# Performance work log

Measured on AMD Instinct MI355X. Metric: run time of the kernel, lower is better.

Reference implementation:

```python
import jax, jax.numpy as jnp
import numpy as np

B, NPG, DIN, ED, DEG = 16, 1024, 16, 8, 32
HEADS, OUT1 = 5, 6
HID = HEADS * OUT1          # 30 features after conv1
C1, C2 = 32, 4              # DIFFPool cluster counts
N = B * NPG                 # 16384 total nodes
E = N * DEG                 # 524288 edges


def _egat_conv(x, src, dst, eattr, W, a_s, a_d, We, heads, outc, n_nodes):
    # Edge-gated GAT: per-edge attention logits from src/dst node features plus
    # a linear projection of edge attributes, segment-softmax over incoming edges.
    h = (x @ W).reshape(n_nodes, heads, outc)
    logit = jax.nn.leaky_relu((h[src] * a_s).sum(-1) + (h[dst] * a_d).sum(-1) + eattr @ We, 0.2)  # [E, heads]
    m = jax.ops.segment_max(logit, dst, num_segments=n_nodes)
    ex = jnp.exp(logit - m[dst])
    den = jax.ops.segment_sum(ex, dst, num_segments=n_nodes)
    alpha = ex / (den[dst] + 1e-16)
    out = jax.ops.segment_sum(alpha[:, :, None] * h[src], dst, num_segments=n_nodes)
    return out.reshape(n_nodes, heads * outc), alpha


def _diff_pool(x, adj, s_logits, b, n, c, d):
    s = jax.nn.softmax(s_logits.reshape(b, n, c), axis=-1)
    xp = jnp.einsum('bnc,bnd->bcd', s, x.reshape(b, n, d))
    adjp = jnp.einsum('bnc,bnm,bmk->bck', s, adj, s)
    reg = jnp.mean((adj - jnp.einsum('bnc,bmc->bnm', s, s)) ** 2)  # link-pred loss
    return xp.reshape(b * c, d), adjp, reg


def _dense_edges(b, c):
    base = jnp.arange(c)
    off = (jnp.arange(b) * c)[:, None]
    src = (jnp.repeat(base, c)[None, :] + off).reshape(-1)
    dst = (jnp.tile(base, c)[None, :] + off).reshape(-1)
    return src, dst


def _forward(x, edge_index, edge_attr, adj, params):
    (W1, a_src1, a_dst1, We1, Wp1, as_p1, ad_p1, Wep1,
     Wp2, as_p2, ad_p2, Wep2, Wf1, bf1, Wf2, bf2) = params
    src, dst = edge_index[0], edge_index[1]
    x1, e = _egat_conv(x, src, dst, edge_attr, W1, a_src1, a_dst1, We1, HEADS, OUT1, N)  # [N,30]
    e_dot = jnp.prod(e, axis=-1)[:, None]  # _EGATConv.dot: product over heads (unused downstream)
    s1, _ = _egat_conv(x1, src, dst, edge_attr, Wp1, as_p1, ad_p1, Wep1, 1, C1, N)
    x2, adj2, reg1 = _diff_pool(x1, adj, s1, B, NPG, C1, HID)
    src2, dst2 = _dense_edges(B, C1)
    ea2 = adj2.reshape(B * C1 * C1, 1)  # pooled graph is dense; adj values as edge attrs
    s2, _ = _egat_conv(x2, src2, dst2, ea2, Wp2, as_p2, ad_p2, Wep2, 1, C2, B * C1)
    x3, _, reg2 = _diff_pool(x2, adj2, s2, B, C1, C2, HID)
    reg = reg1 * 10.0 + reg2 * 0.1
    z = x3.reshape(B, C2 * HID)
    z = jax.nn.relu(z @ Wf1 + bf1)
    logits = z @ Wf2 + bf2
    return logits, reg


def setup_inputs() -> dict:
    key = jax.random.key(0)
    ks = jax.random.split(key, 20)
    # block-diagonal random edges: each graph has NPG*DEG edges within its block
    src_l = jax.random.randint(ks[0], (B, NPG * DEG), 0, NPG)
    dst_l = jax.random.randint(ks[1], (B, NPG * DEG), 0, NPG)
    off = (jnp.arange(B) * NPG)[:, None]
    edge_index = jnp.stack([(src_l + off).reshape(-1), (dst_l + off).reshape(-1)])
    adj = jnp.zeros((B, NPG, NPG), jnp.float32).at[jnp.arange(B)[:, None], src_l, dst_l].set(1.0)
    edge_attr = jax.random.uniform(ks[2], (E, ED), jnp.float32)
    x = jax.random.normal(ks[3], (N, DIN), jnp.float32)
    y = jax.random.randint(ks[4], (B,), 0, 2)

    def nrm(k, shape, fan):
        return jax.random.normal(k, shape, jnp.float32) / np.float32(np.sqrt(fan))

    return dict(
        x=x, edge_index=edge_index, edge_attr=edge_attr, y=y, adj=adj,
        W1=nrm(ks[5], (DIN, HEADS * OUT1), DIN),
        a_src1=nrm(ks[6], (HEADS, OUT1), OUT1),
        a_dst1=nrm(ks[7], (HEADS, OUT1), OUT1),
        We1=nrm(ks[8], (ED, HEADS), ED),
        Wp1=nrm(ks[9], (HID, C1), HID),
        as_p1=nrm(ks[10], (1, C1), C1),
        ad_p1=nrm(ks[11], (1, C1), C1),
        Wep1=nrm(ks[12], (ED, 1), ED),
        Wp2=nrm(ks[13], (HID, C2), HID),
        as_p2=nrm(ks[14], (1, C2), C2),
        ad_p2=nrm(ks[15], (1, C2), C2),
        Wep2=nrm(ks[16], (1, 1), 1),
        Wf1=nrm(ks[17], (C2 * HID, 32), C2 * HID),
        bf1=jnp.zeros((32,), jnp.float32),
        Wf2=nrm(ks[18], (32, 2), 32),
        bf2=jnp.zeros((2,), jnp.float32),
    )


def reference(x, edge_index, edge_attr, y, adj, W1, a_src1, a_dst1, We1, Wp1, as_p1, ad_p1, Wep1, Wp2, as_p2, ad_p2, Wep2, Wf1, bf1, Wf2, bf2):
    params = (W1, a_src1, a_dst1, We1, Wp1, as_p1, ad_p1, Wep1,
              Wp2, as_p2, ad_p2, Wep2, Wf1, bf1, Wf2, bf2)
    return _forward(x, edge_index, edge_attr, adj, params)
```

## Files before the change

kernel.cpp:

```cpp
#include <hip/hip_runtime.h>
#include <math.h>

#define NB 16
#define NPG 1024
#define DIN 16
#define ED 8
#define NHEADS 5
#define OUT1 6
#define HID 30
#define C1 32
#define C2 4
#define NN (NB*NPG)
#define EE (NN*32)
#define EPG 32768
#define CH 16
#define CE 2048

__device__ __forceinline__ float lrelu(float v){ return v >= 0.f ? v : 0.2f*v; }

__device__ __forceinline__ void chunk_gc(int& g, int& c){
    int x = blockIdx.x & 7;
    int j = blockIdx.x >> 3;
    g = x + 8*(j >> 4);
    c = j & 15;
}

__device__ __forceinline__ size_t xcd_chunk_base(){
    int x = blockIdx.x & 7;
    int j = blockIdx.x >> 3;
    int g = x + 8*(j >> 7);
    int c = j & 127;
    return (size_t)g*EPG + (size_t)c*256;
}

__global__ void k_hist_chunk(const int* __restrict__ src, const int* __restrict__ dst,
                             int* __restrict__ histD, int* __restrict__ histS,
                             const float* __restrict__ x, const float* __restrict__ W1,
                             const float* __restrict__ as1, const float* __restrict__ ad1,
                             float* __restrict__ h1, float* __restrict__ hs1, float* __restrict__ hd1){
    int t = threadIdx.x;
    if (blockIdx.x < 256){
        __shared__ int hD[NPG], hS[NPG];
        for (int i = t; i < NPG; i += 256){ hD[i] = 0; hS[i] = 0; }
        __syncthreads();
        int g, c; chunk_gc(g, c);
        size_t e0 = ((size_t)g*CH + c)*CE;
        #pragma unroll
        for (int i = 0; i < 8; i++){
            size_t e = e0 + i*256 + t;
            atomicAdd(&hD[dst[e] & (NPG-1)], 1);
            atomicAdd(&hS[src[e] & (NPG-1)], 1);
        }
        __syncthreads();
        size_t hb = ((size_t)g*CH + c)*NPG;
        for (int i = t; i < NPG; i += 256){
            histD[hb + i] = hD[i];
            histS[hb + i] = hS[i];
        }
        return;
    }
    __shared__ float Ws[DIN*HID];
    __shared__ float as_s[HID], ad_s[HID];
    for (int i = t; i < DIN*HID; i += blockDim.x) Ws[i] = W1[i];
    if (t < HID){ as_s[t] = as1[t]; ad_s[t] = ad1[t]; }
    __syncthreads();
    int n = (blockIdx.x - 256)*blockDim.x + t;
    if (n >= NN) return;
    float xv[DIN];
    #pragma unroll
    for (int i = 0; i < DIN; i++) xv[i] = x[n*DIN + i];
    float hv[HID];
    #pragma unroll
    for (int j = 0; j < HID; j++){
        float a = 0.f;
        #pragma unroll
        for (int i = 0; i < DIN; i++) a += xv[i]*Ws[i*HID + j];
        hv[j] = a; h1[(size_t)n*HID + j] = a;
    }
    #pragma unroll
    for (int h = 0; h < NHEADS; h++){
        float s = 0.f, d = 0.f;
        #pragma unroll
        for (int c2 = 0; c2 < OUT1; c2++){ s += hv[h*OUT1+c2]*as_s[h*OUT1+c2]; d += hv[h*OUT1+c2]*ad_s[h*OUT1+c2]; }
        hs1[n*NHEADS + h] = s; hd1[n*NHEADS + h] = d;
    }
}

__global__ void k_cumhist(int* __restrict__ histD, int* __restrict__ histS,
                          int* __restrict__ deg, int* __restrict__ degS){
    int tid = blockIdx.x*blockDim.x + threadIdx.x;
    int* hist; int* dg;
    if (tid < NN){ hist = histD; dg = deg; }
    else         { hist = histS; dg = degS; tid -= NN; }
    int g = tid >> 10, n = tid & (NPG-1);
    int run = 0;
    #pragma unroll
    for (int c = 0; c < CH; c++){
        size_t idx = ((size_t)g*CH + c)*NPG + n;
        int v = hist[idx];
        hist[idx] = run;
        run += v;
    }
    dg[tid] = run;
}

__global__ __launch_bounds__(1024) void k_scan2f(const int* __restrict__ deg,
                        const int* __restrict__ degS,
                        int* __restrict__ rowptr, int* __restrict__ rowptrS){
    __shared__ int wtot[16];
    __shared__ int wbase[16];
    const int* d = (blockIdx.x == 0) ? deg    : degS;
    int* rp      = (blockIdx.x == 0) ? rowptr : rowptrS;
    int t = threadIdx.x;
    int lane = t & 63, wv = t >> 6;
    int base = t*16;
    int loc[16]; int tot = 0;
    #pragma unroll
    for (int i = 0; i < 16; i++){ loc[i] = tot; tot += d[base + i]; }
    int sincl = tot;
    #pragma unroll
    for (int off = 1; off < 64; off <<= 1){
        int v = __shfl_up(sincl, off, 64);
        if (lane >= off) sincl += v;
    }
    if (lane == 63) wtot[wv] = sincl;
    __syncthreads();
    if (t == 0){
        int run = 0;
        #pragma unroll
        for (int w = 0; w < 16; w++){ wbase[w] = run; run += wtot[w]; }
    }
    __syncthreads();
    int gexcl = wbase[wv] + sincl - tot;
    #pragma unroll
    for (int i = 0; i < 16; i++) rp[base + i] = gexcl + loc[i];
    if (t == 1023) rp[NN] = gexcl + tot;
}

__global__ void k_scatter_det(const int* __restrict__ src, const int* __restrict__ dst,
                              const int* __restrict__ rowptr, const int* __restrict__ rowptrS,
                              const int* __restrict__ histD, const int* __restrict__ histS,
                              int2* __restrict__ se, int* __restrict__ nbrS){
    __shared__ int baseD[NPG], baseS[NPG];
    int t = threadIdx.x;
    int g, c; chunk_gc(g, c);
    size_t hb = ((size_t)g*CH + c)*NPG;
    for (int i = t; i < NPG; i += 256){
        baseD[i] = rowptr[g*NPG + i] + histD[hb + i];
        baseS[i] = rowptrS[g*NPG + i] + histS[hb + i];
    }
    __syncthreads();
    size_t e0 = ((size_t)g*CH + c)*CE;
    #pragma unroll
    for (int i = 0; i < 8; i++){
        size_t e = e0 + i*256 + t;
        int s = src[e], d = dst[e];
        int p = atomicAdd(&baseD[d & (NPG-1)], 1);
        se[p] = make_int2(s, (int)e);
        int pS = atomicAdd(&baseS[s & (NPG-1)], 1);
        nbrS[pS] = d;
    }
}

__global__ void k_elogit(const float* __restrict__ ea, const float* __restrict__ We1,
                         const float* __restrict__ Wep1, const int2* __restrict__ se,
                         const int* __restrict__ dst,
                         const float* __restrict__ hs1, const float* __restrict__ hd1,
                         float* __restrict__ lg1, float* __restrict__ ewp1s){
    __shared__ float W[ED*NHEADS];
    __shared__ float Wp[ED];
    int t = threadIdx.x;
    if (t < ED*NHEADS) W[t] = We1[t];
    if (t < ED) Wp[t] = Wep1[t];
    __syncthreads();
    size_t k = xcd_chunk_base() + t;
    int2 pr = se[k];
    int s = pr.x, e = pr.y;
    int d = dst[e];
    float a[ED];
    #pragma unroll
    for (int i = 0; i < ED; i++) a[i] = ea[(size_t)e*ED + i];
    const float* hsr = hs1 + (size_t)s*NHEADS;
    const float* hdr = hd1 + (size_t)d*NHEADS;
    #pragma unroll
    for (int h = 0; h < NHEADS; h++){
        float sv = 0.f;
        #pragma unroll
        for (int i = 0; i < ED; i++) sv += a[i]*W[i*NHEADS + h];
        lg1[k*NHEADS + h] = lrelu(hsr[h] + hdr[h] + sv);
    }
    float sv = 0.f;
    #pragma unroll
    for (int i = 0; i < ED; i++) sv += a[i]*Wp[i];
    ewp1s[k] = sv;
}

__global__ void k_dedup(const int* __restrict__ rowptrS, const int* __restrict__ nbrS,
                        int* __restrict__ unbr, int* __restrict__ ucnt,
                        float* __restrict__ scal){
    __shared__ unsigned int bm[256*33];
    __shared__ int red[256];
    int t = threadIdx.x;
    unsigned int* mybm = &bm[t*33];
    #pragma unroll
    for (int i = 0; i < 32; i++) mybm[i] = 0u;
    int n = blockIdx.x*blockDim.x + t;
    int cnt = 0;
    if (n < NN){
        int k0 = rowptrS[n], k1 = rowptrS[n+1];
        for (int k = k0; k < k1; k++){
            int m = nbrS[k];
            int loc = m & (NPG-1);
            unsigned int w = (unsigned int)(loc >> 5);
            unsigned int bit = 1u << (loc & 31);
            unsigned int old = mybm[w];
            if (!(old & bit)){
                mybm[w] = old | bit;
                unbr[k0 + cnt] = m;
                cnt++;
            }
        }
        ucnt[n] = cnt;
    }
    red[t] = cnt; __syncthreads();
    for (int s = 128; s > 0; s >>= 1){ if (t < s) red[t] += red[t+s]; __syncthreads(); }
    if (t == 0) atomicAdd(&scal[0], (float)red[0]);
}

__global__ void k_conv1_agg(const int2* __restrict__ se, const int* __restrict__ rowptr,
                            const float* __restrict__ h1, const float* __restrict__ lg1,
                            float* __restrict__ x1){
    int tid = blockIdx.x*blockDim.x + threadIdx.x;
    if (tid >= NN*NHEADS*2) return;
    int n = tid / (NHEADS*2);
    int r = tid - n*(NHEADS*2);
    int h = r >> 1;
    int q = r & 1;
    int k0 = rowptr[n], k1 = rowptr[n+1];
    float m = -INFINITY, den = 0.f;
    float acc[3] = {0.f, 0.f, 0.f};
    int k = k0;
    for (; k + 4 <= k1; k += 4){
        float l0 = lg1[(size_t)(k+0)*NHEADS + h];
        float l1 = lg1[(size_t)(k+1)*NHEADS + h];
        float l2 = lg1[(size_t)(k+2)*NHEADS + h];
        float l3 = lg1[(size_t)(k+3)*NHEADS + h];
        int s0 = se[k+0].x, s1 = se[k+1].x, s2 = se[k+2].x, s3 = se[k+3].x;
        const float* p0 = h1 + (size_t)s0*HID + h*OUT1 + q*3;
        const float* p1 = h1 + (size_t)s1*HID + h*OUT1 + q*3;
        const float* p2 = h1 + (size_t)s2*HID + h*OUT1 + q*3;
        const float* p3 = h1 + (size_t)s3*HID + h*OUT1 + q*3;
        float mb = fmaxf(fmaxf(l0, l1), fmaxf(l2, l3));
        float mn = fmaxf(m, mb);
        float f  = expf(m - mn);
        float e0 = expf(l0 - mn), e1 = expf(l1 - mn);
        float e2 = expf(l2 - mn), e3 = expf(l3 - mn);
        m = mn;
        den = den*f + e0 + e1 + e2 + e3;
        #pragma unroll
        for (int c = 0; c < 3; c++)
            acc[c] = acc[c]*f + e0*p0[c] + e1*p1[c] + e2*p2[c] + e3*p3[c];
    }
    for (; k < k1; k++){
        float l = lg1[(size_t)k*NHEADS + h];
        int s = se[k].x;
        float mn = fmaxf(m, l);
        float f  = expf(m - mn);
        float ex = expf(l - mn);
        m = mn;
        den = den*f + ex;
        const float* hr = h1 + (size_t)s*HID + h*OUT1 + q*3;
        #pragma unroll
        for (int c = 0; c < 3; c++) acc[c] = acc[c]*f + ex*hr[c];
    }
    float inv = 1.f / (den + 1e-16f);
    #pragma unroll
    for (int c = 0; c < 3; c++) x1[(size_t)n*HID + h*OUT1 + q*3 + c] = acc[c]*inv;
}

__global__ void k_node_proj_p1(const float* __restrict__ x1, const float* __restrict__ Wp1,
                               const float* __restrict__ asp, const float* __restrict__ adp,
                               float* __restrict__ hp1, float* __restrict__ hsp, float* __restrict__ hdp){
    __shared__ float Ws[HID*C1];
    __shared__ float as_s[C1], ad_s[C1];
    for (int i = threadIdx.x; i < HID*C1; i += blockDim.x) Ws[i] = Wp1[i];
    if (threadIdx.x < C1){ as_s[threadIdx.x] = asp[threadIdx.x]; ad_s[threadIdx.x] = adp[threadIdx.x]; }
    __syncthreads();
    int n = blockIdx.x*blockDim.x + threadIdx.x;
    if (n >= NN) return;
    float xv[HID];
    #pragma unroll
    for (int d = 0; d < HID; d++) xv[d] = x1[(size_t)n*HID + d];
    float s = 0.f, dd = 0.f;
    for (int c = 0; c < C1; c++){
        float a = 0.f;
        #pragma unroll
        for (int d = 0; d < HID; d++) a += xv[d]*Ws[d*C1 + c];
        hp1[(size_t)n*C1 + c] = a;
        s += a*as_s[c]; dd += a*ad_s[c];
    }
    hsp[n] = s; hdp[n] = dd;
}

__global__ void k_plogit(const int2* __restrict__ se, const int* __restrict__ dst,
                         const float* __restrict__ hsp, const float* __restrict__ hdp,
                         const float* __restrict__ ewp1s, float* __restrict__ lgp){
    size_t k = xcd_chunk_base() + threadIdx.x;
    int2 pr = se[k];
    int d = dst[pr.y];
    lgp[k] = lrelu(hsp[pr.x] + hdp[d] + ewp1s[k]);
}

__global__ void k_pool1_agg(const int2* __restrict__ se, const int* __restrict__ rowptr,
                            const float* __restrict__ hp1, const float* __restrict__ lgp,
                            float* __restrict__ s1){
    int tid = blockIdx.x*blockDim.x + threadIdx.x;
    if (tid >= NN*8) return;
    int q = tid & 7;
    int n = tid >> 3;
    int k0 = rowptr[n], k1 = rowptr[n+1];
    float m = -INFINITY, den = 0.f;
    float acc[4] = {0.f, 0.f, 0.f, 0.f};
    int k = k0;
    for (; k + 4 <= k1; k += 4){
        float l0 = lgp[k+0], l1 = lgp[k+1], l2 = lgp[k+2], l3 = lgp[k+3];
        int s0 = se[k+0].x, s1n = se[k+1].x, s2 = se[k+2].x, s3 = se[k+3].x;
        float4 v0 = *(const float4*)(hp1 + (size_t)s0*C1 + q*4);
        float4 v1 = *(const float4*)(hp1 + (size_t)s1n*C1 + q*4);
        float4 v2 = *(const float4*)(hp1 + (size_t)s2*C1 + q*4);
        float4 v3 = *(const float4*)(hp1 + (size_t)s3*C1 + q*4);
        float mb = fmaxf(fmaxf(l0, l1), fmaxf(l2, l3));
        float mn = fmaxf(m, mb);
        float f  = expf(m - mn);
        float e0 = expf(l0 - mn), e1 = expf(l1 - mn);
        float e2 = expf(l2 - mn), e3 = expf(l3 - mn);
        m = mn;
        den = den*f + e0 + e1 + e2 + e3;
        acc[0] = acc[0]*f + e0*v0.x + e1*v1.x + e2*v2.x + e3*v3.x;
        acc[1] = acc[1]*f + e0*v0.y + e1*v1.y + e2*v2.y + e3*v3.y;
        acc[2] = acc[2]*f + e0*v0.z + e1*v1.z + e2*v2.z + e3*v3.z;
        acc[3] = acc[3]*f + e0*v0.w + e1*v1.w + e2*v2.w + e3*v3.w;
    }
    for (; k < k1; k++){
        float l = lgp[k];
        int s = se[k].x;
        float mn = fmaxf(m, l);
        float f  = expf(m - mn);
        float ex = expf(l - mn);
        m = mn;
        den = den*f + ex;
        const float* hr = hp1 + (size_t)s*C1 + q*4;
        #pragma unroll
        for (int c = 0; c < 4; c++) acc[c] = acc[c]*f + ex*hr[c];
    }
    float inv = 1.f / (den + 1e-16f);
    #pragma unroll
    for (int c = 0; c < 4; c++) s1[(size_t)n*C1 + q*4 + c] = acc[c]*inv;
}

__global__ void k_soft32(const float* __restrict__ s1, float* __restrict__ ssoft){
    int n = blockIdx.x*blockDim.x + threadIdx.x;
    if (n >= NN) return;
    float v[C1];
    float m = -INFINITY;
    #pragma unroll
    for (int c = 0; c < C1; c++){ v[c] = s1[(size_t)n*C1 + c]; m = fmaxf(m, v[c]); }
    float sum = 0.f;
    #pragma unroll
    for (int c = 0; c < C1; c++){ v[c] = expf(v[c] - m); sum += v[c]; }
    float inv = 1.f/sum;
    #pragma unroll
    for (int c = 0; c < C1; c++) ssoft[(size_t)n*C1 + c] = v[c]*inv;
}

__global__ void k_T(const int* __restrict__ rowptrS, const int* __restrict__ unbr,
                    const int* __restrict__ ucnt, const float* __restrict__ ssoft,
                    float* __restrict__ T){
    int tid = blockIdx.x*blockDim.x + threadIdx.x;
    if (tid >= NN*8) return;
    int q = tid & 7;
    int n = tid >> 3;
    int k0 = rowptrS[n];
    int cnt = ucnt[n];
    float acc[4] = {0.f, 0.f, 0.f, 0.f};
    int i = 0;
    for (; i + 4 <= cnt; i += 4){
        int m0 = unbr[k0+i+0], m1 = unbr[k0+i+1], m2 = unbr[k0+i+2], m3 = unbr[k0+i+3];
        float4 v0 = *(const float4*)(ssoft + (size_t)m0*C1 + q*4);
        float4 v1 = *(const float4*)(ssoft + (size_t)m1*C1 + q*4);
        float4 v2 = *(const float4*)(ssoft + (size_t)m2*C1 + q*4);
        float4 v3 = *(const float4*)(ssoft + (size_t)m3*C1 + q*4);
        acc[0] += v0.x + v1.x + v2.x + v3.x;
        acc[1] += v0.y + v1.y + v2.y + v3.y;
        acc[2] += v0.z + v1.z + v2.z + v3.z;
        acc[3] += v0.w + v1.w + v2.w + v3.w;
    }
    for (; i < cnt; i++){
        int m = unbr[k0 + i];
        const float* sr = ssoft + (size_t)m*C1 + q*4;
        #pragma unroll
        for (int c = 0; c < 4; c++) acc[c] += sr[c];
    }
    #pragma unroll
    for (int c = 0; c < 4; c++) T[(size_t)n*C1 + q*4 + c] = acc[c];
}

__global__ void k_partials(const float* __restrict__ ssoft, const float* __restrict__ T,
                           const float* __restrict__ x1,
                           float* __restrict__ adj2, float* __restrict__ Gm,
                           float* __restrict__ x2){
    int b  = blockIdx.y;
    int n0 = blockIdx.x * 64;
    int t  = threadIdx.x;
    __shared__ float ssh[64*C1];
    __shared__ float tsh[64*C1];
    __shared__ float xsh[64*HID];
    {
        size_t sbase = ((size_t)b*NPG + n0)*C1;
        #pragma unroll
        for (int i = 0; i < 8; i++){
            int lin = t + i*256;
            ssh[lin] = ssoft[sbase + lin];
            tsh[lin] = T[sbase + lin];
        }
        size_t xbase = ((size_t)b*NPG + n0)*HID;
        for (int lin = t; lin < 64*HID; lin += 256) xsh[lin] = x1[xbase + lin];
    }
    __syncthreads();
    float accA[4] = {0,0,0,0}, accG[4] = {0,0,0,0}, accX[4] = {0,0,0,0};
    int cA[4], kA[4], cX[4], dX[4];
    #pragma unroll
    for (int q = 0; q < 4; q++){
        int p = t + q*256;
        cA[q] = p >> 5; kA[q] = p & 31;
        cX[q] = p / HID; dX[q] = p - cX[q]*HID;
    }
    for (int r = 0; r < 64; r++){
        const float* sr = ssh + r*C1;
        const float* tr = tsh + r*C1;
        const float* xr = xsh + r*HID;
        #pragma unroll
        for (int q = 0; q < 4; q++){
            float sc = sr[cA[q]];
            accA[q] += sc*tr[kA[q]];
            accG[q] += sc*sr[kA[q]];
        }
        #pragma unroll
        for (int q = 0; q < 4; q++){
            int p = t + q*256;
            if (p < C1*HID) accX[q] += sr[cX[q]]*xr[dX[q]];
        }
    }
    #pragma unroll
    for (int q = 0; q < 4; q++){
        int p = t + q*256;
        atomicAdd(&adj2[(size_t)b*1024 + p], accA[q]);
        atomicAdd(&Gm[(size_t)b*1024 + p], accG[q]);
        if (p < C1*HID) atomicAdd(&x2[((size_t)b*C1 + cX[q])*HID + dX[q]], accX[q]);
    }
}

__global__ void k_tail(const float* __restrict__ x2, const float* __restrict__ adj2,
                       const float* __restrict__ Gm,
                       const float* __restrict__ Wp2, const float* __restrict__ asp,
                       const float* __restrict__ adp, const float* __restrict__ Wep2,
                       const float* __restrict__ Wf1, const float* __restrict__ bf1,
                       const float* __restrict__ Wf2, const float* __restrict__ bf2,
                       float* __restrict__ out, float* __restrict__ scal){
    int b = blockIdx.x;
    int t = threadIdx.x;
    __shared__ float x2s[C1*HID];
    __shared__ float a2s[C1*C1];
    __shared__ float Wps[HID*C2];
    __shared__ float h2s[C1*C2];
    __shared__ float hs2s[C1], hd2s[C1];
    __shared__ float sss[C1*C2];
    __shared__ float x3s[C2*HID];
    __shared__ float zsh[32];
    __shared__ float red[256];
    for (int i = t; i < C1*HID; i += 256) x2s[i] = x2[(size_t)b*C1*HID + i];
    for (int i = t; i < C1*C1; i += 256) a2s[i] = adj2[(size_t)b*C1*C1 + i];
    if (t < HID*C2) Wps[t] = Wp2[t];
    __syncthreads();
    {
        float ltr = 0.f, lfr = 0.f;
        for (int p = t; p < 1024; p += 256){
            float g = Gm[(size_t)b*1024 + p];
            lfr += g*g;
            if ((p >> 5) == (p & 31)) ltr += a2s[p];
        }
        red[t] = ltr; __syncthreads();
        for (int s = 128; s > 0; s >>= 1){ if (t < s) red[t] += red[t+s]; __syncthreads(); }
        if (t == 0) atomicAdd(&scal[1], red[0]);
        __syncthreads();
        red[t] = lfr; __syncthreads();
        for (int s = 128; s > 0; s >>= 1){ if (t < s) red[t] += red[t+s]; __syncthreads(); }
        if (t == 0) atomicAdd(&scal[2], red[0]);
        __syncthreads();
    }
    if (t < C1){
        float s = 0.f, dd = 0.f;
        #pragma unroll
        for (int c = 0; c < C2; c++){
            float a = 0.f;
            #pragma unroll
            for (int d = 0; d < HID; d++) a += x2s[t*HID + d]*Wps[d*C2 + c];
            h2s[t*C2 + c] = a;
            s += a*asp[c]; dd += a*adp[c];
        }
        hs2s[t] = s; hd2s[t] = dd;
    }
    __syncthreads();
    if (t < C1){
        int j = t;
        float hdv = hd2s[j];
        float wep = Wep2[0];
        float m = -INFINITY;
        for (int i = 0; i < C1; i++)
            m = fmaxf(m, lrelu(hs2s[i] + hdv + a2s[i*C1 + j]*wep));
        float den = 0.f;
        float acc[C2] = {0,0,0,0};
        for (int i = 0; i < C1; i++){
            float ex = expf(lrelu(hs2s[i] + hdv + a2s[i*C1 + j]*wep) - m);
            den += ex;
            #pragma unroll
            for (int c = 0; c < C2; c++) acc[c] += ex * h2s[i*C2 + c];
        }
        float inv = 1.f/(den + 1e-16f);
        float v[C2]; float mx = -INFINITY;
        #pragma unroll
        for (int c = 0; c < C2; c++){ v[c] = acc[c]*inv; mx = fmaxf(mx, v[c]); }
        float sum = 0.f;
        #pragma unroll
        for (int c = 0; c < C2; c++){ v[c] = expf(v[c] - mx); sum += v[c]; }
        float i2 = 1.f/sum;
        #pragma unroll
        for (int c = 0; c < C2; c++) sss[j*C2 + c] = v[c]*i2;
    }
    __syncthreads();
    if (t < C2*HID){
        int c = t / HID, d = t % HID;
        float a = 0.f;
        #pragma unroll
        for (int n = 0; n < C1; n++) a += sss[n*C2 + c]*x2s[n*HID + d];
        x3s[t] = a;
    }
    {
        float loc = 0.f;
        for (int p = t; p < 1024; p += 256){
            int n = p >> 5, mm = p & 31;
            float dot = 0.f;
            #pragma unroll
            for (int c = 0; c < C2; c++) dot += sss[n*C2 + c]*sss[mm*C2 + c];
            float df = a2s[p] - dot;
            loc += df*df;
        }
        red[t] = loc; __syncthreads();
        for (int s = 128; s > 0; s >>= 1){ if (t < s) red[t] += red[t+s]; __syncthreads(); }
        if (t == 0) atomicAdd(&scal[3], red[0]);
        __syncthreads();
    }
    if (t < 32){
        float a = bf1[t];
        #pragma unroll 4
        for (int k = 0; k < C2*HID; k++) a += x3s[k]*Wf1[k*32 + t];
        zsh[t] = fmaxf(a, 0.f);
    }
    __syncthreads();
    if (t < 2){
        float a = bf2[t];
        #pragma unroll
        for (int j = 0; j < 32; j++) a += zsh[j]*Wf2[j*2 + t];
        out[b*2 + t] = a;
    }
}

__global__ void k_reg(const float* __restrict__ scal, float* __restrict__ out){
    if (threadIdx.x == 0){
        float adjsum = scal[0], tr = scal[1], fr = scal[2], r2 = scal[3];
        float reg1 = (adjsum - 2.f*tr + fr) * (1.f/16777216.f);
        float reg2 = r2 * (1.f/16384.f);
        out[32] = 10.f*reg1 + 0.1f*reg2;
    }
}

extern "C" void kernel_launch(void* const* d_in, const int* in_sizes, int n_in,
                              void* d_out, int out_size, void* d_ws, size_t ws_size,
                              hipStream_t stream) {
    const float* x    = (const float*)d_in[0];
    const int*   ei   = (const int*)d_in[1];
    const float* ea   = (const float*)d_in[2];
    const float* W1   = (const float*)d_in[5];
    const float* as1  = (const float*)d_in[6];
    const float* ad1  = (const float*)d_in[7];
    const float* We1  = (const float*)d_in[8];
    const float* Wp1  = (const float*)d_in[9];
    const float* asp1 = (const float*)d_in[10];
    const float* adp1 = (const float*)d_in[11];
    const float* Wep1 = (const float*)d_in[12];
    const float* Wp2  = (const float*)d_in[13];
    const float* asp2 = (const float*)d_in[14];
    const float* adp2 = (const float*)d_in[15];
    const float* Wep2 = (const float*)d_in[16];
    const float* Wf1  = (const float*)d_in[17];
    const float* bf1  = (const float*)d_in[18];
    const float* Wf2  = (const float*)d_in[19];
    const float* bf2  = (const float*)d_in[20];
    float* out = (float*)d_out;

    const int* srcA = ei;
    const int* dstA = ei + EE;

    char* wp = (char*)d_ws;
    auto carve = [&](size_t bytes)->char*{
        char* p = wp;
        wp += (bytes + 255) & ~(size_t)255;
        return p;
    };
    float* h1    = (float*)carve((size_t)NN*HID*4);
    float* hs1   = (float*)carve((size_t)NN*NHEADS*4);
    float* hd1   = (float*)carve((size_t)NN*NHEADS*4);
    float* lg1   = (float*)carve((size_t)EE*NHEADS*4);
    float* ewp1s = (float*)carve((size_t)EE*4);
    float* lgp   = (float*)carve((size_t)EE*4);
    float* x1    = (float*)carve((size_t)NN*HID*4);
    float* hp1   = (float*)carve((size_t)NN*C1*4);
    float* hsp   = (float*)carve((size_t)NN*4);
    float* hdp   = (float*)carve((size_t)NN*4);
    float* s1    = (float*)carve((size_t)NN*C1*4);
    float* ssoft = (float*)carve((size_t)NN*C1*4);
    float* T     = (float*)carve((size_t)NN*C1*4);
    float* x2    = (float*)carve((size_t)NB*C1*HID*4);
    float* adj2  = (float*)carve((size_t)NB*C1*C1*4);
    float* Gm    = (float*)carve((size_t)NB*C1*C1*4);
    float* scal  = (float*)carve(16*4);
    int* histD   = (int*)carve((size_t)NB*CH*NPG*4);
    int* histS   = (int*)carve((size_t)NB*CH*NPG*4);
    int* deg     = (int*)carve((size_t)NN*4);
    int* degS    = (int*)carve((size_t)NN*4);
    int* rowptr  = (int*)carve((size_t)(NN+1)*4);
    int* rowptrS = (int*)carve((size_t)(NN+1)*4);
    int2* se     = (int2*)carve((size_t)EE*8);
    int* nbrS    = (int*)carve((size_t)EE*4);
    int* unbr    = (int*)carve((size_t)EE*4);
    int* ucnt    = (int*)carve((size_t)NN*4);

    hipMemsetAsync(scal, 0, 16*4, stream);
    hipMemsetAsync(x2, 0, (size_t)(NB*C1*HID + 2*NB*C1*C1)*4, stream);

    const int TB = 256;
    dim3 gN((NN + TB - 1)/TB);

    k_hist_chunk<<<dim3(256 + 64), TB, 0, stream>>>(srcA, dstA, histD, histS,
                                                    x, W1, as1, ad1, h1, hs1, hd1);
    k_cumhist<<<dim3(128), TB, 0, stream>>>(histD, histS, deg, degS);
    k_scan2f<<<dim3(2), 1024, 0, stream>>>(deg, degS, rowptr, rowptrS);
    k_scatter_det<<<dim3(256), TB, 0, stream>>>(srcA, dstA, rowptr, rowptrS,
                                                histD, histS, se, nbrS);

    k_elogit<<<dim3(2048), TB, 0, stream>>>(ea, We1, Wep1, se, dstA, hs1, hd1, lg1, ewp1s);
    k_dedup<<<dim3(NN/TB), TB, 0, stream>>>(rowptrS, nbrS, unbr, ucnt, scal);

    k_conv1_agg<<<dim3(NN*NHEADS*2/TB), TB, 0, stream>>>(se, rowptr, h1, lg1, x1);

    k_node_proj_p1<<<gN, TB, 0, stream>>>(x1, Wp1, asp1, adp1, hp1, hsp, hdp);
    k_plogit<<<dim3(2048), TB, 0, stream>>>(se, dstA, hsp, hdp, ewp1s, lgp);
    k_pool1_agg<<<dim3(NN*8/TB), TB, 0, stream>>>(se, rowptr, hp1, lgp, s1);

    k_soft32<<<gN, TB, 0, stream>>>(s1, ssoft);
    k_T<<<dim3(NN*8/TB), TB, 0, stream>>>(rowptrS, unbr, ucnt, ssoft, T);
    k_partials<<<dim3(16, NB), TB, 0, stream>>>(ssoft, T, x1, adj2, Gm, x2);

    k_tail<<<dim3(NB), TB, 0, stream>>>(x2, adj2, Gm, Wp2, asp2, adp2, Wep2,
                                        Wf1, bf1, Wf2, bf2, out, scal);

    k_reg<<<1, 64, 0, stream>>>(scal, out);
}
```

Baseline: 288.2 us.

## Fuse scan kernels, split edge arrays, transpose logits, fuse pool softmax

Merges the per-chunk histogram prefix and the global row-pointer scan into one kernel that uses a fixed per-graph edge offset, which removes a launch and the deg buffers. The interleaved (src, eid) array is split into separate src, eid and dst arrays so later kernels stop gathering dst through the edge id. Attention logits are stored head-major so each aggregation thread reads them contiguously. The 32-way cluster softmax is folded into the pool aggregation through shared memory, which drops a kernel and an intermediate buffer. The fixed per-graph offset assumes exactly EPG edges per graph, and the split arrays add one extra write stream in the scatter.

```diff
diff --git a/kernel.cpp b/kernel.cpp
--- a/kernel.cpp
+++ b/kernel.cpp
@@ -86,38 +86,24 @@
     }
 }
 
-__global__ void k_cumhist(int* __restrict__ histD, int* __restrict__ histS,
-                          int* __restrict__ deg, int* __restrict__ degS){
-    int tid = blockIdx.x*blockDim.x + threadIdx.x;
-    int* hist; int* dg;
-    if (tid < NN){ hist = histD; dg = deg; }
-    else         { hist = histS; dg = degS; tid -= NN; }
-    int g = tid >> 10, n = tid & (NPG-1);
+__global__ __launch_bounds__(1024) void k_cumscan(int* __restrict__ histD, int* __restrict__ histS,
+                                                  int* __restrict__ rowptr, int* __restrict__ rowptrS){
+    __shared__ int wtot[16], wbase[16];
+    bool isD = (blockIdx.x < NB);
+    int b = isD ? blockIdx.x : (blockIdx.x - NB);
+    int* hist = isD ? histD : histS;
+    int* rp   = isD ? rowptr : rowptrS;
+    int n = threadIdx.x;
     int run = 0;
     #pragma unroll
     for (int c = 0; c < CH; c++){
-        size_t idx = ((size_t)g*CH + c)*NPG + n;
+        size_t idx = ((size_t)b*CH + c)*NPG + n;
         int v = hist[idx];
         hist[idx] = run;
         run += v;
     }
-    dg[tid] = run;
-}
-
-__global__ __launch_bounds__(1024) void k_scan2f(const int* __restrict__ deg,
-                        const int* __restrict__ degS,
-                        int* __restrict__ rowptr, int* __restrict__ rowptrS){
-    __shared__ int wtot[16];
-    __shared__ int wbase[16];
-    const int* d = (blockIdx.x == 0) ? deg    : degS;
-    int* rp      = (blockIdx.x == 0) ? rowptr : rowptrS;
-    int t = threadIdx.x;
-    int lane = t & 63, wv = t >> 6;
-    int base = t*16;
-    int loc[16]; int tot = 0;
-    #pragma unroll
-    for (int i = 0; i < 16; i++){ loc[i] = tot; tot += d[base + i]; }
-    int sincl = tot;
+    int lane = n & 63, wv = n >> 6;
+    int sincl = run;
     #pragma unroll
     for (int off = 1; off < 64; off <<= 1){
         int v = __shfl_up(sincl, off, 64);
@@ -125,22 +111,22 @@
     }
     if (lane == 63) wtot[wv] = sincl;
     __syncthreads();
-    if (t == 0){
-        int run = 0;
-        #pragma unroll
-        for (int w = 0; w < 16; w++){ wbase[w] = run; run += wtot[w]; }
-    }
-    __syncthreads();
-    int gexcl = wbase[wv] + sincl - tot;
-    #pragma unroll
-    for (int i = 0; i < 16; i++) rp[base + i] = gexcl + loc[i];
-    if (t == 1023) rp[NN] = gexcl + tot;
+    if (n == 0){
+        int r = 0;
+        #pragma unroll
+        for (int w = 0; w < 16; w++){ wbase[w] = r; r += wtot[w]; }
+    }
+    __syncthreads();
+    int excl = wbase[wv] + sincl - run;
+    rp[b*NPG + n] = b*EPG + excl;
+    if (b == NB-1 && n == NPG-1) rp[NN] = EE;
 }
 
 __global__ void k_scatter_det(const int* __restrict__ src, const int* __restrict__ dst,
                               const int* __restrict__ rowptr, const int* __restrict__ rowptrS,
                               const int* __restrict__ histD, const int* __restrict__ histS,
-                              int2* __restrict__ se, int* __restrict__ nbrS){
+                              int* __restrict__ srcs, int* __restrict__ eid,
+                              int* __restrict__ dsts, int* __restrict__ nbrS){
     __shared__ int baseD[NPG], baseS[NPG];
     int t = threadIdx.x;
     int g, c; chunk_gc(g, c);
@@ -156,17 +142,18 @@
         size_t e = e0 + i*256 + t;
         int s = src[e], d = dst[e];
         int p = atomicAdd(&baseD[d & (NPG-1)], 1);
-        se[p] = make_int2(s, (int)e);
+        srcs[p] = s; eid[p] = (int)e; dsts[p] = d;
         int pS = atomicAdd(&baseS[s & (NPG-1)], 1);
         nbrS[pS] = d;
     }
 }
 
 __global__ void k_elogit(const float* __restrict__ ea, const float* __restrict__ We1,
-                         const float* __restrict__ Wep1, const int2* __restrict__ se,
-                         const int* __restrict__ dst,
+                         const float* __restrict__ Wep1,
+                         const int* __restrict__ srcs, const int* __restrict__ eid,
+                         const int* __restrict__ dsts,
                          const float* __restrict__ hs1, const float* __restrict__ hd1,
-                         float* __restrict__ lg1, float* __restrict__ ewp1s){
+                         float* __restrict__ lg1T, float* __restrict__ ewp1s){
     __shared__ float W[ED*NHEADS];
     __shared__ float Wp[ED];
     int t = threadIdx.x;
@@ -174,9 +161,7 @@
     if (t < ED) Wp[t] = Wep1[t];
     __syncthreads();
     size_t k = xcd_chunk_base() + t;
-    int2 pr = se[k];
-    int s = pr.x, e = pr.y;
-    int d = dst[e];
+    int s = srcs[k], e = eid[k], d = dsts[k];
     float a[ED];
     #pragma unroll
     for (int i = 0; i < ED; i++) a[i] = ea[(size_t)e*ED + i];
@@ -187,7 +172,7 @@
         float sv = 0.f;
         #pragma unroll
         for (int i = 0; i < ED; i++) sv += a[i]*W[i*NHEADS + h];
-        lg1[k*NHEADS + h] = lrelu(hsr[h] + hdr[h] + sv);
+        lg1T[(size_t)h*EE + k] = lrelu(hsr[h] + hdr[h] + sv);
     }
     float sv = 0.f;
     #pragma unroll
@@ -227,8 +212,8 @@
     if (t == 0) atomicAdd(&scal[0], (float)red[0]);
 }
 
-__global__ void k_conv1_agg(const int2* __restrict__ se, const int* __restrict__ rowptr,
-                            const float* __restrict__ h1, const float* __restrict__ lg1,
+__global__ void k_conv1_agg(const int* __restrict__ srcs, const int* __restrict__ rowptr,
+                            const float* __restrict__ h1, const float* __restrict__ lg1T,
                             float* __restrict__ x1){
     int tid = blockIdx.x*blockDim.x + threadIdx.x;
     if (tid >= NN*NHEADS*2) return;
@@ -237,15 +222,13 @@
     int h = r >> 1;
     int q = r & 1;
     int k0 = rowptr[n], k1 = rowptr[n+1];
+    const float* lgh = lg1T + (size_t)h*EE;
     float m = -INFINITY, den = 0.f;
     float acc[3] = {0.f, 0.f, 0.f};
     int k = k0;
     for (; k + 4 <= k1; k += 4){
-        float l0 = lg1[(size_t)(k+0)*NHEADS + h];
-        float l1 = lg1[(size_t)(k+1)*NHEADS + h];
-        float l2 = lg1[(size_t)(k+2)*NHEADS + h];
-        float l3 = lg1[(size_t)(k+3)*NHEADS + h];
-        int s0 = se[k+0].x, s1 = se[k+1].x, s2 = se[k+2].x, s3 = se[k+3].x;
+        float l0 = lgh[k+0], l1 = lgh[k+1], l2 = lgh[k+2], l3 = lgh[k+3];
+        int s0 = srcs[k+0], s1 = srcs[k+1], s2 = srcs[k+2], s3 = srcs[k+3];
         const float* p0 = h1 + (size_t)s0*HID + h*OUT1 + q*3;
         const float* p1 = h1 + (size_t)s1*HID + h*OUT1 + q*3;
         const float* p2 = h1 + (size_t)s2*HID + h*OUT1 + q*3;
@@ -262,8 +245,8 @@
             acc[c] = acc[c]*f + e0*p0[c] + e1*p1[c] + e2*p2[c] + e3*p3[c];
     }
     for (; k < k1; k++){
-        float l = lg1[(size_t)k*NHEADS + h];
-        int s = se[k].x;
+        float l = lgh[k];
+        int s = srcs[k];
         float mn = fmaxf(m, l);
         float f  = expf(m - mn);
         float ex = expf(l - mn);
@@ -302,29 +285,28 @@
     hsp[n] = s; hdp[n] = dd;
 }
 
-__global__ void k_plogit(const int2* __restrict__ se, const int* __restrict__ dst,
+__global__ void k_plogit(const int* __restrict__ srcs, const int* __restrict__ dsts,
                          const float* __restrict__ hsp, const float* __restrict__ hdp,
                          const float* __restrict__ ewp1s, float* __restrict__ lgp){
     size_t k = xcd_chunk_base() + threadIdx.x;
-    int2 pr = se[k];
-    int d = dst[pr.y];
-    lgp[k] = lrelu(hsp[pr.x] + hdp[d] + ewp1s[k]);
-}
-
-__global__ void k_pool1_agg(const int2* __restrict__ se, const int* __restrict__ rowptr,
+    lgp[k] = lrelu(hsp[srcs[k]] + hdp[dsts[k]] + ewp1s[k]);
+}
+
+__global__ void k_pool1_agg(const int* __restrict__ srcs, const int* __restrict__ rowptr,
                             const float* __restrict__ hp1, const float* __restrict__ lgp,
-                            float* __restrict__ s1){
+                            float* __restrict__ ssoft){
+    __shared__ float sm[32*33];
     int tid = blockIdx.x*blockDim.x + threadIdx.x;
-    if (tid >= NN*8) return;
     int q = tid & 7;
     int n = tid >> 3;
+    int nl = threadIdx.x >> 3;
     int k0 = rowptr[n], k1 = rowptr[n+1];
     float m = -INFINITY, den = 0.f;
     float acc[4] = {0.f, 0.f, 0.f, 0.f};
     int k = k0;
     for (; k + 4 <= k1; k += 4){
         float l0 = lgp[k+0], l1 = lgp[k+1], l2 = lgp[k+2], l3 = lgp[k+3];
-        int s0 = se[k+0].x, s1n = se[k+1].x, s2 = se[k+2].x, s3 = se[k+3].x;
+        int s0 = srcs[k+0], s1n = srcs[k+1], s2 = srcs[k+2], s3 = srcs[k+3];
         float4 v0 = *(const float4*)(hp1 + (size_t)s0*C1 + q*4);
         float4 v1 = *(const float4*)(hp1 + (size_t)s1n*C1 + q*4);
         float4 v2 = *(const float4*)(hp1 + (size_t)s2*C1 + q*4);
@@ -343,7 +325,7 @@
     }
     for (; k < k1; k++){
         float l = lgp[k];
-        int s = se[k].x;
+        int s = srcs[k];
         float mn = fmaxf(m, l);
         float f  = expf(m - mn);
         float ex = expf(l - mn);
@@ -355,22 +337,18 @@
     }
     float inv = 1.f / (den + 1e-16f);
     #pragma unroll
-    for (int c = 0; c < 4; c++) s1[(size_t)n*C1 + q*4 + c] = acc[c]*inv;
-}
-
-__global__ void k_soft32(const float* __restrict__ s1, float* __restrict__ ssoft){
-    int n = blockIdx.x*blockDim.x + threadIdx.x;
-    if (n >= NN) return;
-    float v[C1];
-    float m = -INFINITY;
-    #pragma unroll
-    for (int c = 0; c < C1; c++){ v[c] = s1[(size_t)n*C1 + c]; m = fmaxf(m, v[c]); }
+    for (int c = 0; c < 4; c++) sm[nl*33 + q*4 + c] = acc[c]*inv;
+    __syncthreads();
+    float mx = -INFINITY;
+    #pragma unroll 8
+    for (int i = 0; i < C1; i++) mx = fmaxf(mx, sm[nl*33 + i]);
     float sum = 0.f;
-    #pragma unroll
-    for (int c = 0; c < C1; c++){ v[c] = expf(v[c] - m); sum += v[c]; }
-    float inv = 1.f/sum;
-    #pragma unroll
-    for (int c = 0; c < C1; c++) ssoft[(size_t)n*C1 + c] = v[c]*inv;
+    #pragma unroll 8
+    for (int i = 0; i < C1; i++) sum += expf(sm[nl*33 + i] - mx);
+    float is = 1.f/sum;
+    #pragma unroll
+    for (int c = 0; c < 4; c++)
+        ssoft[(size_t)n*C1 + q*4 + c] = expf(sm[nl*33 + q*4 + c] - mx)*is;
 }
 
 __global__ void k_T(const int* __restrict__ rowptrS, const int* __restrict__ unbr,
@@ -620,14 +598,13 @@
     float* h1    = (float*)carve((size_t)NN*HID*4);
     float* hs1   = (float*)carve((size_t)NN*NHEADS*4);
     float* hd1   = (float*)carve((size_t)NN*NHEADS*4);
-    float* lg1   = (float*)carve((size_t)EE*NHEADS*4);
+    float* lg1T  = (float*)carve((size_t)EE*NHEADS*4);
     float* ewp1s = (float*)carve((size_t)EE*4);
     float* lgp   = (float*)carve((size_t)EE*4);
     float* x1    = (float*)carve((size_t)NN*HID*4);
     float* hp1   = (float*)carve((size_t)NN*C1*4);
     float* hsp   = (float*)carve((size_t)NN*4);
     float* hdp   = (float*)carve((size_t)NN*4);
-    float* s1    = (float*)carve((size_t)NN*C1*4);
     float* ssoft = (float*)carve((size_t)NN*C1*4);
     float* T     = (float*)carve((size_t)NN*C1*4);
     float* x2    = (float*)carve((size_t)NB*C1*HID*4);
@@ -636,11 +613,11 @@
     float* scal  = (float*)carve(16*4);
     int* histD   = (int*)carve((size_t)NB*CH*NPG*4);
     int* histS   = (int*)carve((size_t)NB*CH*NPG*4);
-    int* deg     = (int*)carve((size_t)NN*4);
-    int* degS    = (int*)carve((size_t)NN*4);
     int* rowptr  = (int*)carve((size_t)(NN+1)*4);
     int* rowptrS = (int*)carve((size_t)(NN+1)*4);
-    int2* se     = (int2*)carve((size_t)EE*8);
+    int* srcs    = (int*)carve((size_t)EE*4);
+    int* eid     = (int*)carve((size_t)EE*4);
+    int* dsts    = (int*)carve((size_t)EE*4);
     int* nbrS    = (int*)carve((size_t)EE*4);
     int* unbr    = (int*)carve((size_t)EE*4);
     int* ucnt    = (int*)carve((size_t)NN*4);
@@ -653,21 +630,19 @@
 
     k_hist_chunk<<<dim3(256 + 64), TB, 0, stream>>>(srcA, dstA, histD, histS,
                                                     x, W1, as1, ad1, h1, hs1, hd1);
-    k_cumhist<<<dim3(128), TB, 0, stream>>>(histD, histS, deg, degS);
-    k_scan2f<<<dim3(2), 1024, 0, stream>>>(deg, degS, rowptr, rowptrS);
+    k_cumscan<<<dim3(2*NB), 1024, 0, stream>>>(histD, histS, rowptr, rowptrS);
     k_scatter_det<<<dim3(256), TB, 0, stream>>>(srcA, dstA, rowptr, rowptrS,
-                                                histD, histS, se, nbrS);
-
-    k_elogit<<<dim3(2048), TB, 0, stream>>>(ea, We1, Wep1, se, dstA, hs1, hd1, lg1, ewp1s);
+                                                histD, histS, srcs, eid, dsts, nbrS);
+
+    k_elogit<<<dim3(2048), TB, 0, stream>>>(ea, We1, Wep1, srcs, eid, dsts, hs1, hd1, lg1T, ewp1s);
     k_dedup<<<dim3(NN/TB), TB, 0, stream>>>(rowptrS, nbrS, unbr, ucnt, scal);
 
-    k_conv1_agg<<<dim3(NN*NHEADS*2/TB), TB, 0, stream>>>(se, rowptr, h1, lg1, x1);
+    k_conv1_agg<<<dim3(NN*NHEADS*2/TB), TB, 0, stream>>>(srcs, rowptr, h1, lg1T, x1);
 
     k_node_proj_p1<<<gN, TB, 0, stream>>>(x1, Wp1, asp1, adp1, hp1, hsp, hdp);
-    k_plogit<<<dim3(2048), TB, 0, stream>>>(se, dstA, hsp, hdp, ewp1s, lgp);
-    k_pool1_agg<<<dim3(NN*8/TB), TB, 0, stream>>>(se, rowptr, hp1, lgp, s1);
-
-    k_soft32<<<gN, TB, 0, stream>>>(s1, ssoft);
+    k_plogit<<<dim3(2048), TB, 0, stream>>>(srcs, dsts, hsp, hdp, ewp1s, lgp);
+    k_pool1_agg<<<dim3(NN*8/TB), TB, 0, stream>>>(srcs, rowptr, hp1, lgp, ssoft);
+
     k_T<<<dim3(NN*8/TB), TB, 0, stream>>>(rowptrS, unbr, ucnt, ssoft, T);
     k_partials<<<dim3(16, NB), TB, 0, stream>>>(ssoft, T, x1, adj2, Gm, x2);
 
```

New measurement: 290.7 us. About the same (+0.9%).
